# Kernel tuning notes

Measured on AMD Instinct MI355X. Metric: run time of the kernel, lower is better.

## Reference

```python
import jax, jax.numpy as jnp
import numpy as np

N_RES = 4096
BATCH = 1024
N_IN = 128
N_OUT = 64
TEACHER_SHIFT = 0.0
TEACHER_SCALE = 1.0
PREV_STATE_WEIGHT = 0.1
SPECTRAL_RADIUS = 0.95


def setup_inputs() -> dict:
    key = jax.random.key(0)
    ks = jax.random.split(key, 9)
    # Reservoir weights, scaled to fixed spectral radius (as in build()).
    W_res = jax.random.uniform(ks[0], (N_RES, N_RES), minval=-0.5, maxval=0.5, dtype=jnp.float32)
    e = jnp.linalg.eigvalsh(W_res)  # tf.linalg.eigh also treats matrix as symmetric
    W_res = W_res * (SPECTRAL_RADIUS / jnp.max(jnp.abs(e)))
    W_in = jax.random.uniform(ks[1], (N_RES, N_IN), minval=-1.0, maxval=1.0, dtype=jnp.float32)
    W_out = jax.random.uniform(ks[2], (N_RES, N_OUT), minval=-1.0, maxval=1.0, dtype=jnp.float32)
    B_in = 0.1 * jax.random.normal(ks[3], (N_RES, 1), dtype=jnp.float32)
    return {
        "passed": jax.random.normal(ks[4], (BATCH, N_IN), dtype=jnp.float32),
        "lastOutput": jax.random.normal(ks[5], (N_OUT, BATCH), dtype=jnp.float32),
        "lastPredOutput": jax.random.normal(ks[6], (N_OUT, BATCH), dtype=jnp.float32),
        "x": jax.random.normal(ks[7], (BATCH, N_RES), dtype=jnp.float32),
        "prob": 50.0 * jnp.ones((1,), dtype=jnp.float32),
        "rand_num": jax.random.uniform(ks[8], (1,), minval=1.0, maxval=100.0, dtype=jnp.float32),
        "W_in": W_in,
        "W_res": W_res,
        "W_out": W_out,
        "B_in": B_in,
    }


def reference(passed, lastOutput, lastPredOutput, x, prob, rand_num, W_in, W_res, W_out, B_in):
    # Teacher forcing selection (tf.case on random draw vs prob), applied after scale/shift.
    last_true = lastOutput * TEACHER_SCALE + TEACHER_SHIFT      # [n_out, B]
    last_pred = lastPredOutput * TEACHER_SCALE + TEACHER_SHIFT  # [n_out, B]
    toUse = jnp.where(rand_num[0] < prob[0], last_true, last_pred)  # [n_out, B]

    # Batched version of the per-sample loop:
    #   tanh(W_in@u_i + W_res@x_i + W_out@toUse[:,i] + B_in)
    pre = (passed @ W_in.T            # [B, N] input drive
           + x @ W_res.T              # [B, N] recurrent drive
           + toUse.T @ W_out.T        # [B, N] output feedback
           + B_in[:, 0][None, :])     # [1, N] bias
    new_state = PREV_STATE_WEIGHT * x + (1.0 - PREV_STATE_WEIGHT) * jnp.tanh(pre)
    return new_state  # [B, N]; original returns this split into B [1,N] tensors
```

## Files before the change

kernel.cpp:

```cpp
#include <hip/hip_runtime.h>
#include <hip/hip_bf16.h>
#include <math.h>

#define NRES   4096
#define NBATCH 1024
#define NIN    128
#define NOUT   64
#define KT     4672
#define KQ     (KT / 4)
#define TILES  73
#define MN     ((size_t)NBATCH * NRES)

typedef __bf16 bf16x8 __attribute__((ext_vector_type(8)));
typedef __bf16 bf16x4 __attribute__((ext_vector_type(4)));
typedef float  f32x4  __attribute__((ext_vector_type(4)));

__device__ __forceinline__ float lo_part(float f) {
    return f - (float)(__bf16)f;
}

__device__ __forceinline__ void gload_lds16(const __bf16* g, __bf16* l) {
    __builtin_amdgcn_global_load_lds(
        (const __attribute__((address_space(1))) unsigned int*)g,
        (__attribute__((address_space(3))) unsigned int*)l, 16, 0, 0);
}

__global__ __launch_bounds__(256) void pack_A4(
    const float* __restrict__ x, const float* __restrict__ passed,
    const float* __restrict__ lastOut, const float* __restrict__ lastPred,
    const float* __restrict__ prob, const float* __restrict__ rand_num,
    __bf16* __restrict__ Abuf)
{
    unsigned id = blockIdx.x * 256u + threadIdx.x;
    if (id >= (unsigned)NBATCH * KQ) return;
    unsigned b = id / KQ;
    unsigned k = (id - b * KQ) * 4u;
    f32x4 v;
    if (k < 4096u) {
        v = *(const f32x4*)(x + (size_t)b * NRES + k);
    } else if (k < 4224u) {
        v = *(const f32x4*)(passed + b * NIN + (k - 4096u));
    } else if (k < 4352u) {
        v = *(const f32x4*)(passed + b * NIN + (k - 4224u));
    } else if (k < 4480u) {
        f32x4 f = *(const f32x4*)(passed + b * NIN + (k - 4352u));
#pragma unroll
        for (int e = 0; e < 4; ++e) v[e] = lo_part(f[e]);
    } else {
        const float* src = (rand_num[0] < prob[0]) ? lastOut : lastPred;
#pragma unroll
        for (int e = 0; e < 4; ++e) {
            unsigned kk = k + e;
            unsigned j; bool want_lo;
            if (kk < 4544u)      { j = kk - 4480u; want_lo = false; }
            else if (kk < 4608u) { j = kk - 4544u; want_lo = false; }
            else                 { j = kk - 4608u; want_lo = true;  }
            float f = src[j * NBATCH + b];
            v[e] = want_lo ? lo_part(f) : f;
        }
    }
    bf16x4 o;
#pragma unroll
    for (int e = 0; e < 4; ++e) o[e] = (__bf16)v[e];
    *(bf16x4*)(Abuf + (size_t)id * 4u) = o;
}

__global__ __launch_bounds__(256) void pack_B4(
    const float* __restrict__ W_res, const float* __restrict__ W_in,
    const float* __restrict__ W_out, __bf16* __restrict__ Bbuf)
{
    unsigned id = blockIdx.x * 256u + threadIdx.x;
    if (id >= (unsigned)NRES * KQ) return;
    unsigned n = id / KQ;
    unsigned k = (id - n * KQ) * 4u;
    f32x4 v;
    if (k < 4096u) {
        v = *(const f32x4*)(W_res + (size_t)n * NRES + k);
    } else if (k < 4224u) {
        v = *(const f32x4*)(W_in + n * NIN + (k - 4096u));
    } else if (k < 4352u) {
        f32x4 f = *(const f32x4*)(W_in + n * NIN + (k - 4224u));
#pragma unroll
        for (int e = 0; e < 4; ++e) v[e] = lo_part(f[e]);
    } else if (k < 4480u) {
        v = *(const f32x4*)(W_in + n * NIN + (k - 4352u));
    } else if (k < 4544u) {
        v = *(const f32x4*)(W_out + n * NOUT + (k - 4480u));
    } else if (k < 4608u) {
        f32x4 f = *(const f32x4*)(W_out + n * NOUT + (k - 4544u));
#pragma unroll
        for (int e = 0; e < 4; ++e) v[e] = lo_part(f[e]);
    } else {
        v = *(const f32x4*)(W_out + n * NOUT + (k - 4608u));
    }
    bf16x4 o;
#pragma unroll
    for (int e = 0; e < 4; ++e) o[e] = (__bf16)v[e];
    *(bf16x4*)(Bbuf + (size_t)id * 4u) = o;
}

__global__ __launch_bounds__(512, 1) void gemm_kernel(
    const __bf16* __restrict__ Abuf, const __bf16* __restrict__ Bbuf,
    float* __restrict__ part, int split)
{
    __shared__ __align__(16) __bf16 SH[2][32768];

    const int t  = threadIdx.x;
    const int l  = t & 63;
    const int w  = t >> 6;
    const int wm = w >> 2;
    const int wn = w & 3;

    const int nwg  = gridDim.x * gridDim.y * gridDim.z;
    const int cpx  = nwg >> 3;
    const int flat = blockIdx.x + gridDim.x * (blockIdx.y + gridDim.y * blockIdx.z);
    const int o    = (flat & 7) * cpx + (flat >> 3);
    const int bn   = o % gridDim.x;
    const int bm   = (o / gridDim.x) % gridDim.y;
    const int bz   = o / (gridDim.x * gridDim.y);

    const int qs = TILES / split, rs = TILES % split;
    const int t0 = bz * qs + (bz < rs ? bz : rs);
    const int nt = qs + (bz < rs ? 1 : 0);

    f32x4 acc[8][4] = {};

    unsigned goff[4][2];
    int lE[4][2];
#pragma unroll
    for (int c = 0; c < 4; ++c) {
#pragma unroll
        for (int j = 0; j < 2; ++j) {
            int ui = j * 512 + t;
            int lr = ui >> 3;
            int cb = (ui & 7) << 4;
            int rc;
            if (c == 0)      rc = (lr & 63) + ((lr >> 6) << 7);
            else if (c == 1) rc = 64 + (lr & 63) + ((lr >> 6) << 7);
            else if (c == 2) rc = (lr & 31) + ((lr >> 5) << 6);
            else             rc = 32 + (lr & 31) + ((lr >> 5) << 6);
            int cs = cb ^ ((rc & 7) << 4);
            if (c < 2) {
                goff[c][j] = (unsigned)((bm * 256 + rc) * KT) + (cs >> 1);
                lE[c][j]   = rc * 64 + (cb >> 1);
            } else {
                goff[c][j] = (unsigned)((bn * 256 + rc) * KT) + (cs >> 1);
                lE[c][j]   = 16384 + rc * 64 + (cb >> 1);
            }
        }
    }

#define STAGEC(c, nxt, k0n)                                              \
    do {                                                                 \
        gload_lds16(((c) < 2 ? Abuf : Bbuf) + goff[c][0] + (k0n),        \
                    &SH[nxt][lE[c][0]]);                                 \
        gload_lds16(((c) < 2 ? Abuf : Bbuf) + goff[c][1] + (k0n),        \
                    &SH[nxt][lE[c][1]]);                                 \
    } while (0)

    int eA[8], eB[4];
#pragma unroll
    for (int m = 0; m < 8; ++m) {
        int row = wm * 128 + m * 16 + (l & 15);
        eA[m] = row * 64 + (((((l >> 4) << 4)) ^ ((row & 7) << 4)) >> 1);
    }
#pragma unroll
    for (int n = 0; n < 4; ++n) {
        int col = wn * 64 + n * 16 + (l & 15);
        eB[n] = 16384 + col * 64 + (((((l >> 4) << 4)) ^ ((col & 7) << 4)) >> 1);
    }

    bf16x8 af[4][2], bfr[4][2];

#define BAR() do { asm volatile("" ::: "memory");                        \
                   __builtin_amdgcn_s_barrier();                         \
                   asm volatile("" ::: "memory"); } while (0)
#define VM(n) asm volatile("s_waitcnt vmcnt(" #n ")" ::: "memory")

#define LDA(qd, buf)                                                     \
    do {                                                                 \
        _Pragma("unroll")                                                \
        for (int m2 = 0; m2 < 4; ++m2) {                                 \
            af[m2][0] = *(const bf16x8*)&SH[buf][eA[(qd)*4 + m2]];       \
            af[m2][1] = *(const bf16x8*)&SH[buf][eA[(qd)*4 + m2] ^ 32];  \
        }                                                                \
    } while (0)

#define LDB(h, buf)                                                      \
    do {                                                                 \
        _Pragma("unroll")                                                \
        for (int n3 = 0; n3 < 2; ++n3) {                                 \
            bfr[(h)*2+n3][0] = *(const bf16x8*)&SH[buf][eB[(h)*2 + n3]]; \
            bfr[(h)*2+n3][1] = *(const bf16x8*)&SH[buf][eB[(h)*2+n3] ^ 32]; \
        }                                                                \
    } while (0)

#define MFMA16(qm, qn)                                                   \
    do {                                                                 \
        __builtin_amdgcn_s_setprio(1);                                   \
        _Pragma("unroll")                                                \
        for (int kk2 = 0; kk2 < 2; ++kk2)                                \
            _Pragma("unroll")                                            \
            for (int m2 = 0; m2 < 4; ++m2)                               \
                _Pragma("unroll")                                        \
                for (int n2 = 0; n2 < 2; ++n2)                           \
                    acc[(qm)*4+m2][(qn)*2+n2] =                          \
                        __builtin_amdgcn_mfma_f32_16x16x32_bf16(         \
                            af[m2][kk2], bfr[(qn)*2+n2][kk2],            \
                            acc[(qm)*4+m2][(qn)*2+n2], 0, 0, 0);         \
        __builtin_amdgcn_s_setprio(0);                                   \
    } while (0)

    {
        const int k00 = t0 * 64;
        STAGEC(0, 0, k00); STAGEC(2, 0, k00); STAGEC(3, 0, k00); STAGEC(1, 0, k00);
        VM(4);
        BAR();
    }

    for (int tt = 0; tt < nt - 1; ++tt) {
        const int cur = tt & 1;
        const int nxt = cur ^ 1;
        const int k0n = (t0 + tt + 1) * 64;
        LDA(0, cur); LDB(0, cur);
        STAGEC(0, nxt, k0n);
        VM(4);
        BAR();
        MFMA16(0, 0);
        BAR();
        LDB(1, cur);
        STAGEC(2, nxt, k0n);
        VM(4);
        BAR();
        MFMA16(0, 1);
        BAR();
        LDA(1, cur);
        STAGEC(3, nxt, k0n);
        BAR();
        MFMA16(1, 0);
        BAR();
        STAGEC(1, nxt, k0n);
        VM(4);
        BAR();
        MFMA16(1, 1);
        BAR();
    }
    {
        const int cur = (nt - 1) & 1;
        LDA(0, cur); LDB(0, cur);
        VM(2);
        BAR();
        MFMA16(0, 0);
        BAR();
        LDB(1, cur);
        VM(0);
        BAR();
        MFMA16(0, 1);
        BAR();
        LDA(1, cur);
        BAR();
        MFMA16(1, 0);
        BAR();
        MFMA16(1, 1);
    }

    float* pz = part + (size_t)bz * MN;
    const int r0 = bm * 256 + wm * 128 + ((l >> 4) << 2);
    const int c0 = bn * 256 + wn * 64 + (l & 15);
#pragma unroll
    for (int m = 0; m < 8; ++m) {
#pragma unroll
        for (int i = 0; i < 4; ++i) {
            float* prow = pz + (size_t)(r0 + m * 16 + i) * NRES;
#pragma unroll
            for (int n = 0; n < 4; ++n)
                prow[c0 + n * 16] = acc[m][n][i];
        }
    }
#undef STAGEC
#undef BAR
#undef VM
#undef LDA
#undef LDB
#undef MFMA16
}

__global__ __launch_bounds__(256) void epilogue_kernel(
    const float* __restrict__ part, int split, const float* __restrict__ xin,
    const float* __restrict__ Bin, float* __restrict__ out)
{
    size_t id = (size_t)blockIdx.x * 256u + threadIdx.x;
    size_t e  = id * 4;
    int c = (int)(e & (NRES - 1));
    f32x4 s = *(const f32x4*)(part + e);
    for (int z = 1; z < split; ++z) {
        f32x4 p = *(const f32x4*)(part + (size_t)z * MN + e);
        s += p;
    }
    f32x4 xv = *(const f32x4*)(xin + e);
    f32x4 bv = *(const f32x4*)(Bin + c);
    f32x4 o;
#pragma unroll
    for (int j = 0; j < 4; ++j)
        o[j] = 0.1f * xv[j] + 0.9f * tanhf(s[j] + bv[j]);
    *(f32x4*)(out + e) = o;
}

extern "C" void kernel_launch(void* const* d_in, const int* in_sizes, int n_in,
                              void* d_out, int out_size, void* d_ws, size_t ws_size,
                              hipStream_t stream) {
    (void)in_sizes; (void)n_in; (void)out_size;
    const float* passed     = (const float*)d_in[0];
    const float* lastOutput = (const float*)d_in[1];
    const float* lastPred   = (const float*)d_in[2];
    const float* x          = (const float*)d_in[3];
    const float* prob       = (const float*)d_in[4];
    const float* rand_num   = (const float*)d_in[5];
    const float* W_in       = (const float*)d_in[6];
    const float* W_res      = (const float*)d_in[7];
    const float* W_out      = (const float*)d_in[8];
    const float* B_in       = (const float*)d_in[9];
    float* out = (float*)d_out;

    const size_t AB = (size_t)(NBATCH + NRES) * KT * 2;
    __bf16* Abuf = (__bf16*)d_ws;
    __bf16* Bbuf = (__bf16*)((char*)d_ws + (size_t)NBATCH * KT * 2);
    float*  part = (float*)((char*)d_ws + AB);

    int split = 1;
    if (ws_size >= AB + 4 * MN * sizeof(float))      split = 4;
    else if (ws_size >= AB + 2 * MN * sizeof(float)) split = 2;

    pack_A4<<<(NBATCH * KQ) / 256, 256, 0, stream>>>(
        x, passed, lastOutput, lastPred, prob, rand_num, Abuf);
    pack_B4<<<(NRES * KQ) / 256, 256, 0, stream>>>(
        W_res, W_in, W_out, Bbuf);

    dim3 grid(NRES / 256, NBATCH / 256, split);
    gemm_kernel<<<grid, 512, 0, stream>>>(Abuf, Bbuf, part, split);

    epilogue_kernel<<<4096, 256, 0, stream>>>(part, split, x, B_in, out);
}
```

Baseline: 85.94 us.

## Read fp32 x and W_res directly in GEMM, converting to bf16 in registers

Drops the full bf16 repack of x and W_res. The GEMM now loads fp32 tiles straight from the original arrays into registers, converts them to bf16 and writes them to LDS, replacing the direct global-to-LDS bf16 loads. Only the small passed/feedback tail (with its hi/lo split) is still packed, now kept in fp32. This removes the pack pass over about 80 MB of input and its bf16 writes, at the cost of twice the global bytes per tile in the GEMM plus extra register pressure and conversion work inside the main loop.

```diff
diff --git a/kernel.cpp b/kernel.cpp
--- a/kernel.cpp
+++ b/kernel.cpp
@@ -6,101 +6,77 @@
 #define NBATCH 1024
 #define NIN    128
 #define NOUT   64
-#define KT     4672
-#define KQ     (KT / 4)
+#define KTAIL  576
 #define TILES  73
+#define MAINT  64
 #define MN     ((size_t)NBATCH * NRES)
 
 typedef __bf16 bf16x8 __attribute__((ext_vector_type(8)));
-typedef __bf16 bf16x4 __attribute__((ext_vector_type(4)));
 typedef float  f32x4  __attribute__((ext_vector_type(4)));
 
 __device__ __forceinline__ float lo_part(float f) {
     return f - (float)(__bf16)f;
 }
 
-__device__ __forceinline__ void gload_lds16(const __bf16* g, __bf16* l) {
-    __builtin_amdgcn_global_load_lds(
-        (const __attribute__((address_space(1))) unsigned int*)g,
-        (__attribute__((address_space(3))) unsigned int*)l, 16, 0, 0);
-}
-
-__global__ __launch_bounds__(256) void pack_A4(
-    const float* __restrict__ x, const float* __restrict__ passed,
-    const float* __restrict__ lastOut, const float* __restrict__ lastPred,
-    const float* __restrict__ prob, const float* __restrict__ rand_num,
-    __bf16* __restrict__ Abuf)
+__global__ __launch_bounds__(256) void pack_Atail(
+    const float* __restrict__ passed, const float* __restrict__ lastOut,
+    const float* __restrict__ lastPred, const float* __restrict__ prob,
+    const float* __restrict__ rand_num, float* __restrict__ Atail)
 {
     unsigned id = blockIdx.x * 256u + threadIdx.x;
-    if (id >= (unsigned)NBATCH * KQ) return;
-    unsigned b = id / KQ;
-    unsigned k = (id - b * KQ) * 4u;
+    unsigned b  = id / 144u;
+    unsigned c  = (id - b * 144u) * 4u;
     f32x4 v;
-    if (k < 4096u) {
-        v = *(const f32x4*)(x + (size_t)b * NRES + k);
-    } else if (k < 4224u) {
-        v = *(const f32x4*)(passed + b * NIN + (k - 4096u));
-    } else if (k < 4352u) {
-        v = *(const f32x4*)(passed + b * NIN + (k - 4224u));
-    } else if (k < 4480u) {
-        f32x4 f = *(const f32x4*)(passed + b * NIN + (k - 4352u));
+    if (c < 256u) {
+        v = *(const f32x4*)(passed + b * NIN + (c & 127u));
+    } else if (c < 384u) {
+        f32x4 f = *(const f32x4*)(passed + b * NIN + (c - 256u));
 #pragma unroll
         for (int e = 0; e < 4; ++e) v[e] = lo_part(f[e]);
     } else {
         const float* src = (rand_num[0] < prob[0]) ? lastOut : lastPred;
+        bool wlo = (c >= 512u);
+        unsigned j0 = wlo ? (c - 512u) : ((c - 384u) & 63u);
 #pragma unroll
         for (int e = 0; e < 4; ++e) {
-            unsigned kk = k + e;
-            unsigned j; bool want_lo;
-            if (kk < 4544u)      { j = kk - 4480u; want_lo = false; }
-            else if (kk < 4608u) { j = kk - 4544u; want_lo = false; }
-            else                 { j = kk - 4608u; want_lo = true;  }
-            float f = src[j * NBATCH + b];
-            v[e] = want_lo ? lo_part(f) : f;
+            float f = src[(j0 + e) * NBATCH + b];
+            v[e] = wlo ? lo_part(f) : f;
         }
     }
-    bf16x4 o;
-#pragma unroll
-    for (int e = 0; e < 4; ++e) o[e] = (__bf16)v[e];
-    *(bf16x4*)(Abuf + (size_t)id * 4u) = o;
-}
-
-__global__ __launch_bounds__(256) void pack_B4(
-    const float* __restrict__ W_res, const float* __restrict__ W_in,
-    const float* __restrict__ W_out, __bf16* __restrict__ Bbuf)
+    *(f32x4*)(Atail + (size_t)b * KTAIL + c) = v;
+}
+
+__global__ __launch_bounds__(256) void pack_Btail(
+    const float* __restrict__ W_in, const float* __restrict__ W_out,
+    float* __restrict__ Btail)
 {
     unsigned id = blockIdx.x * 256u + threadIdx.x;
-    if (id >= (unsigned)NRES * KQ) return;
-    unsigned n = id / KQ;
-    unsigned k = (id - n * KQ) * 4u;
+    unsigned n  = id / 144u;
+    unsigned c  = (id - n * 144u) * 4u;
     f32x4 v;
-    if (k < 4096u) {
-        v = *(const f32x4*)(W_res + (size_t)n * NRES + k);
-    } else if (k < 4224u) {
-        v = *(const f32x4*)(W_in + n * NIN + (k - 4096u));
-    } else if (k < 4352u) {
-        f32x4 f = *(const f32x4*)(W_in + n * NIN + (k - 4224u));
+    if (c < 128u) {
+        v = *(const f32x4*)(W_in + n * NIN + c);
+    } else if (c < 256u) {
+        f32x4 f = *(const f32x4*)(W_in + n * NIN + (c - 128u));
 #pragma unroll
         for (int e = 0; e < 4; ++e) v[e] = lo_part(f[e]);
-    } else if (k < 4480u) {
-        v = *(const f32x4*)(W_in + n * NIN + (k - 4352u));
-    } else if (k < 4544u) {
-        v = *(const f32x4*)(W_out + n * NOUT + (k - 4480u));
-    } else if (k < 4608u) {
-        f32x4 f = *(const f32x4*)(W_out + n * NOUT + (k - 4544u));
+    } else if (c < 384u) {
+        v = *(const f32x4*)(W_in + n * NIN + (c - 256u));
+    } else if (c < 448u) {
+        v = *(const f32x4*)(W_out + n * NOUT + (c - 384u));
+    } else if (c < 512u) {
+        f32x4 f = *(const f32x4*)(W_out + n * NOUT + (c - 448u));
 #pragma unroll
         for (int e = 0; e < 4; ++e) v[e] = lo_part(f[e]);
     } else {
-        v = *(const f32x4*)(W_out + n * NOUT + (k - 4608u));
-    }
-    bf16x4 o;
-#pragma unroll
-    for (int e = 0; e < 4; ++e) o[e] = (__bf16)v[e];
-    *(bf16x4*)(Bbuf + (size_t)id * 4u) = o;
+        v = *(const f32x4*)(W_out + n * NOUT + (c - 512u));
+    }
+    *(f32x4*)(Btail + (size_t)n * KTAIL + c) = v;
 }
 
 __global__ __launch_bounds__(512, 1) void gemm_kernel(
-    const __bf16* __restrict__ Abuf, const __bf16* __restrict__ Bbuf,
+    const float* __restrict__ xp, const float* __restrict__ wp,
+    const float* __restrict__ atp, const float* __restrict__ btp,
     float* __restrict__ part, int split)
 {
     __shared__ __align__(16) __bf16 SH[2][32768];
@@ -125,38 +101,25 @@
 
     f32x4 acc[8][4] = {};
 
-    unsigned goff[4][2];
-    int lE[4][2];
-#pragma unroll
-    for (int c = 0; c < 4; ++c) {
-#pragma unroll
-        for (int j = 0; j < 2; ++j) {
-            int ui = j * 512 + t;
-            int lr = ui >> 3;
-            int cb = (ui & 7) << 4;
-            int rc;
-            if (c == 0)      rc = (lr & 63) + ((lr >> 6) << 7);
-            else if (c == 1) rc = 64 + (lr & 63) + ((lr >> 6) << 7);
-            else if (c == 2) rc = (lr & 31) + ((lr >> 5) << 6);
-            else             rc = 32 + (lr & 31) + ((lr >> 5) << 6);
-            int cs = cb ^ ((rc & 7) << 4);
-            if (c < 2) {
-                goff[c][j] = (unsigned)((bm * 256 + rc) * KT) + (cs >> 1);
-                lE[c][j]   = rc * 64 + (cb >> 1);
-            } else {
-                goff[c][j] = (unsigned)((bn * 256 + rc) * KT) + (cs >> 1);
-                lE[c][j]   = 16384 + rc * 64 + (cb >> 1);
-            }
-        }
-    }
-
-#define STAGEC(c, nxt, k0n)                                              \
-    do {                                                                 \
-        gload_lds16(((c) < 2 ? Abuf : Bbuf) + goff[c][0] + (k0n),        \
-                    &SH[nxt][lE[c][0]]);                                 \
-        gload_lds16(((c) < 2 ? Abuf : Bbuf) + goff[c][1] + (k0n),        \
-                    &SH[nxt][lE[c][1]]);                                 \
-    } while (0)
+    const int lr = t >> 2;
+    const int u  = t & 3;
+    const int rcA0 = (lr & 63) + ((lr >> 6) << 7);
+    const int rcA1 = rcA0 + 64;
+    const int rcB0 = (lr & 31) + ((lr >> 5) << 6);
+    const int rcB1 = rcB0 + 32;
+    const size_t u16 = (size_t)(u * 16);
+    const size_t pAm0 = (size_t)(bm * 256 + rcA0) * NRES  + u16;
+    const size_t pAm1 = (size_t)(bm * 256 + rcA1) * NRES  + u16;
+    const size_t pAt0 = (size_t)(bm * 256 + rcA0) * KTAIL + u16;
+    const size_t pAt1 = (size_t)(bm * 256 + rcA1) * KTAIL + u16;
+    const size_t pBm0 = (size_t)(bn * 256 + rcB0) * NRES  + u16;
+    const size_t pBm1 = (size_t)(bn * 256 + rcB1) * NRES  + u16;
+    const size_t pBt0 = (size_t)(bn * 256 + rcB0) * KTAIL + u16;
+    const size_t pBt1 = (size_t)(bn * 256 + rcB1) * KTAIL + u16;
+    const int elWA0 = rcA0 * 64 + ((u * 16) ^ ((rcA0 & 7) * 8));
+    const int elWA1 = rcA1 * 64 + ((u * 16) ^ ((rcA1 & 7) * 8));
+    const int elWB0 = 16384 + rcB0 * 64 + ((u * 16) ^ ((rcB0 & 7) * 8));
+    const int elWB1 = 16384 + rcB1 * 64 + ((u * 16) ^ ((rcB1 & 7) * 8));
 
     int eA[8], eB[4];
 #pragma unroll
@@ -170,12 +133,41 @@
         eB[n] = 16384 + col * 64 + (((((l >> 4) << 4)) ^ ((col & 7) << 4)) >> 1);
     }
 
+    f32x4 sa0, sa1, sa2, sa3;
+    f32x4 sb0, sb1, sb2, sb3;
     bf16x8 af[4][2], bfr[4][2];
 
 #define BAR() do { asm volatile("" ::: "memory");                        \
                    __builtin_amdgcn_s_barrier();                         \
                    asm volatile("" ::: "memory"); } while (0)
 #define VM(n) asm volatile("s_waitcnt vmcnt(" #n ")" ::: "memory")
+#define LG0() asm volatile("s_waitcnt lgkmcnt(0)" ::: "memory")
+
+#define ISS(BK, msrc, tsrc, pm, pt, ktv)                                 \
+    do {                                                                 \
+        const float* bp_ = ((ktv) < MAINT)                               \
+            ? (msrc) + (pm) + (size_t)(ktv) * 64                         \
+            : (tsrc) + (pt) + (size_t)((ktv) - MAINT) * 64;              \
+        BK##0 = *(const f32x4*)(bp_);                                    \
+        BK##1 = *(const f32x4*)(bp_ + 4);                                \
+        BK##2 = *(const f32x4*)(bp_ + 8);                                \
+        BK##3 = *(const f32x4*)(bp_ + 12);                               \
+    } while (0)
+
+#define WRT(BK, eloff, buf)                                              \
+    do {                                                                 \
+        bf16x8 w0_, w1_;                                                 \
+        w0_[0]=(__bf16)BK##0[0]; w0_[1]=(__bf16)BK##0[1];                \
+        w0_[2]=(__bf16)BK##0[2]; w0_[3]=(__bf16)BK##0[3];                \
+        w0_[4]=(__bf16)BK##1[0]; w0_[5]=(__bf16)BK##1[1];                \
+        w0_[6]=(__bf16)BK##1[2]; w0_[7]=(__bf16)BK##1[3];                \
+        w1_[0]=(__bf16)BK##2[0]; w1_[1]=(__bf16)BK##2[1];                \
+        w1_[2]=(__bf16)BK##2[2]; w1_[3]=(__bf16)BK##2[3];                \
+        w1_[4]=(__bf16)BK##3[0]; w1_[5]=(__bf16)BK##3[1];                \
+        w1_[6]=(__bf16)BK##3[2]; w1_[7]=(__bf16)BK##3[3];                \
+        *(bf16x8*)&SH[buf][(eloff)]     = w0_;                           \
+        *(bf16x8*)&SH[buf][(eloff) ^ 8] = w1_;                           \
+    } while (0)
 
 #define LDA(qd, buf)                                                     \
     do {                                                                 \
@@ -212,48 +204,65 @@
     } while (0)
 
     {
-        const int k00 = t0 * 64;
-        STAGEC(0, 0, k00); STAGEC(2, 0, k00); STAGEC(3, 0, k00); STAGEC(1, 0, k00);
-        VM(4);
+        const int kt0 = t0;
+        ISS(sa, xp, atp, pAm0, pAt0, kt0);
+        ISS(sb, wp, btp, pBm0, pBt0, kt0);
+        VM(4);
+        WRT(sa, elWA0, 0);
+        ISS(sa, wp, btp, pBm1, pBt1, kt0);
+        VM(4);
+        WRT(sb, elWB0, 0);
+        LG0();
         BAR();
     }
 
     for (int tt = 0; tt < nt - 1; ++tt) {
         const int cur = tt & 1;
         const int nxt = cur ^ 1;
-        const int k0n = (t0 + tt + 1) * 64;
+        const int kt  = t0 + tt;
+        const int ktn = kt + 1;
+        ISS(sb, xp, atp, pAm1, pAt1, kt);
+        VM(4);
+        WRT(sa, elWB1, cur);
         LDA(0, cur); LDB(0, cur);
-        STAGEC(0, nxt, k0n);
-        VM(4);
         BAR();
         MFMA16(0, 0);
         BAR();
+        ISS(sa, xp, atp, pAm0, pAt0, ktn);
+        VM(4);
+        WRT(sb, elWA1, cur);
         LDB(1, cur);
-        STAGEC(2, nxt, k0n);
-        VM(4);
         BAR();
         MFMA16(0, 1);
         BAR();
+        ISS(sb, wp, btp, pBm0, pBt0, ktn);
+        VM(4);
+        WRT(sa, elWA0, nxt);
         LDA(1, cur);
-        STAGEC(3, nxt, k0n);
         BAR();
         MFMA16(1, 0);
         BAR();
-        STAGEC(1, nxt, k0n);
-        VM(4);
+        ISS(sa, wp, btp, pBm1, pBt1, ktn);
+        VM(4);
+        WRT(sb, elWB0, nxt);
+        LG0();
         BAR();
         MFMA16(1, 1);
         BAR();
     }
     {
         const int cur = (nt - 1) & 1;
+        const int kt  = t0 + nt - 1;
+        ISS(sb, xp, atp, pAm1, pAt1, kt);
+        VM(4);
+        WRT(sa, elWB1, cur);
         LDA(0, cur); LDB(0, cur);
-        VM(2);
         BAR();
         MFMA16(0, 0);
         BAR();
+        VM(0);
+        WRT(sb, elWA1, cur);
         LDB(1, cur);
-        VM(0);
         BAR();
         MFMA16(0, 1);
         BAR();
@@ -277,9 +286,11 @@
                 prow[c0 + n * 16] = acc[m][n][i];
         }
     }
-#undef STAGEC
 #undef BAR
 #undef VM
+#undef LG0
+#undef ISS
+#undef WRT
 #undef LDA
 #undef LDB
 #undef MFMA16
@@ -322,22 +333,23 @@
     const float* B_in       = (const float*)d_in[9];
     float* out = (float*)d_out;
 
-    const size_t AB = (size_t)(NBATCH + NRES) * KT * 2;
-    __bf16* Abuf = (__bf16*)d_ws;
-    __bf16* Bbuf = (__bf16*)((char*)d_ws + (size_t)NBATCH * KT * 2);
-    float*  part = (float*)((char*)d_ws + AB);
+    const size_t ATB = (size_t)NBATCH * KTAIL * 4;
+    const size_t BTB = (size_t)NRES   * KTAIL * 4;
+    float* Atail = (float*)d_ws;
+    float* Btail = (float*)((char*)d_ws + ATB);
+    float* part  = (float*)((char*)d_ws + ATB + BTB);
 
     int split = 1;
-    if (ws_size >= AB + 4 * MN * sizeof(float))      split = 4;
-    else if (ws_size >= AB + 2 * MN * sizeof(float)) split = 2;
-
-    pack_A4<<<(NBATCH * KQ) / 256, 256, 0, stream>>>(
-        x, passed, lastOutput, lastPred, prob, rand_num, Abuf);
-    pack_B4<<<(NRES * KQ) / 256, 256, 0, stream>>>(
-        W_res, W_in, W_out, Bbuf);
+    if (ws_size >= ATB + BTB + 4 * MN * sizeof(float))      split = 4;
+    else if (ws_size >= ATB + BTB + 2 * MN * sizeof(float)) split = 2;
+
+    pack_Atail<<<(NBATCH * (KTAIL / 4)) / 256, 256, 0, stream>>>(
+        passed, lastOutput, lastPred, prob, rand_num, Atail);
+    pack_Btail<<<(NRES * (KTAIL / 4)) / 256, 256, 0, stream>>>(
+        W_in, W_out, Btail);
 
     dim3 grid(NRES / 256, NBATCH / 256, split);
-    gemm_kernel<<<grid, 512, 0, stream>>>(Abuf, Bbuf, part, split);
+    gemm_kernel<<<grid, 512, 0, stream>>>(x, W_res, Atail, Btail, part, split);
 
     epilogue_kernel<<<4096, 256, 0, stream>>>(part, split, x, B_in, out);
 }
```

Result: faster. 83.44 us (-2.9%).
